# Optimization experiments

Hardware: AMD Instinct MI355X
Metric: run time of the kernel (lower is better)

Reference implementation:

```python
import jax, jax.numpy as jnp
import numpy as np

B = 32; NMAX = 256; E = 512; H = 512; U = 256; M = 32; L = 2; P = 4; TAU = 1.0
S = NMAX + 1                      # pseudo-seq len = nodes + SOS
IN0 = E + (M - 1) + P             # GRU layer-0 input size


def setup_inputs() -> dict:
    key = jax.random.key(0)
    ks = jax.random.split(key, 22)
    f = lambda k, sh, sc=0.05: jax.random.normal(k, sh, dtype=jnp.float32) * sc
    return {
        "h_padded": jax.random.normal(ks[0], (B, NMAX, E), jnp.float32),
        "hg": jax.random.normal(ks[1], (B, E), jnp.float32),
        "num_nodes": jax.random.randint(ks[2], (B,), 1, NMAX + 1),
        "u_noise": jax.random.uniform(ks[3], (M, B, S), jnp.float32),
        "emb_special": f(ks[4], (2, E), 1.0),
        "emb_pos": f(ks[5], (M, P), 1.0),
        "Wp": f(ks[6], (L * H, E)), "bp": f(ks[7], (L * H,)),
        "W_ih0": f(ks[8], (3 * H, IN0)), "W_hh0": f(ks[9], (3 * H, H)),
        "b_ih0": f(ks[10], (3 * H,)), "b_hh0": f(ks[11], (3 * H,)),
        "W_ih1": f(ks[12], (3 * H, H)), "W_hh1": f(ks[13], (3 * H, H)),
        "b_ih1": f(ks[14], (3 * H,)), "b_hh1": f(ks[15], (3 * H,)),
        "W1": f(ks[16], (U, H)), "W2": f(ks[17], (U, H)),
        "wc": f(ks[18], (U,)), "V": f(ks[19], (U,)),
        "Wf": f(ks[20], (M - 1, H)), "bf": f(ks[21], (M - 1,)),
    }


def _gru_step(x, hid, params):
    # torch nn.GRU single time step, L layers; gate order (r, z, n)
    new = []
    inp = x
    for l, (Wi, Wh, bi, bh) in enumerate(params):
        hp = hid[l]
        gi = inp @ Wi.T + bi
        gh = hp @ Wh.T + bh
        gi_r, gi_z, gi_n = jnp.split(gi, 3, axis=-1)
        gh_r, gh_z, gh_n = jnp.split(gh, 3, axis=-1)
        r = jax.nn.sigmoid(gi_r + gh_r)
        z = jax.nn.sigmoid(gi_z + gh_z)
        n = jnp.tanh(gi_n + r * gh_n)
        hn = (1.0 - z) * n + z * hp
        new.append(hn)
        inp = hn
    return inp, jnp.stack(new, 0)


def reference(h_padded, hg, num_nodes, u_noise, emb_special, emb_pos, Wp, bp,
              W_ih0, W_hh0, b_ih0, b_hh0, W_ih1, W_hh1, b_ih1, b_hh1,
              W1, W2, wc, V, Wf, bf):
    lens = num_nodes + 1
    mask = jnp.arange(S)[None, :] < lens[:, None]                       # [B,S]
    node_valid = (jnp.arange(NMAX)[None, :] < num_nodes[:, None]).astype(h_padded.dtype)
    # encoder_out = [SOS emb ; h nodes ; zero pad] as pad_sequence would give
    sos_enc = jnp.broadcast_to(emb_special[1], (B, 1, E))
    encoder_out = jnp.concatenate([sos_enc, h_padded * node_valid[..., None]], axis=1)  # [B,S,E]
    enc_W1 = encoder_out @ W1.T                                          # [B,S,U] hoisted (loop-invariant)
    dec_hidden = jnp.tanh(hg @ Wp.T + bp).reshape(B, L, H).transpose(1, 0, 2)  # [L,B,H]
    theta0 = jnp.zeros((B, M - 1), encoder_out.dtype)
    dec_input = jnp.concatenate([jnp.broadcast_to(emb_special[0], (B, E)), theta0], axis=1)
    cov_vec0 = jnp.zeros((B, S), encoder_out.dtype)
    gumbel = -jnp.log(-jnp.log(u_noise + 1e-10) + 1e-10)                 # [M,B,S]
    gru_params = ((W_ih0, W_hh0, b_ih0, b_hh0), (W_ih1, W_hh1, b_ih1, b_hh1))
    neg = jnp.float32(-1e30)

    def step(carry, xs):
        dec_in, hid, cov_vec, cov_loss = carry
        i, pe, g = xs
        x = jnp.concatenate([dec_in, jnp.broadcast_to(pe, (B, P))], axis=1)
        out, hid = _gru_step(x, hid, gru_params)                        # out [B,H]
        # Bahdanau attention with coverage
        uj = enc_W1 + (out @ W2.T)[:, None, :] + cov_vec[..., None] * wc
        uj = jnp.tanh(uj) @ V                                           # [B,S]
        aj = jax.nn.softmax(jnp.where(mask, uj, neg), axis=-1)
        # hard gumbel-softmax (straight-through)
        logits = jnp.log(aj + 1e-12)
        y = jax.nn.softmax((logits + g) / TAU, axis=1)
        onehot = jax.nn.one_hot(jnp.argmax(y, axis=1), S, dtype=y.dtype)
        hard = jax.lax.stop_gradient(onehot - y) + y
        chosen = jnp.einsum('bse,bs->be', encoder_out, hard)            # [B,E]
        cov_loss = cov_loss + jnp.minimum(aj, cov_vec).sum()
        cov_vec = cov_vec + aj
        theta = jnp.where(i < 1,
                          jnp.zeros((B, M - 1), out.dtype),
                          jax.nn.sigmoid(out @ Wf.T + bf))
        dec_next = jnp.concatenate([chosen, theta], axis=1)
        return (dec_next, hid, cov_vec, cov_loss), (hard, theta, aj)

    init = (dec_input, dec_hidden, cov_vec0, jnp.float32(0.0))
    xs = (jnp.arange(M), emb_pos, gumbel)
    carry_f, (hards, thetas, ajs) = jax.lax.scan(step, init, xs)
    cov_loss = carry_f[3] / B
    pointer = jnp.transpose(hards, (1, 2, 0))   # [B,S,M]
    adj = jnp.transpose(thetas, (1, 2, 0))      # [B,M-1,M]
    atts = jnp.transpose(ajs, (1, 2, 0))        # [B,S,M]
    return pointer, cov_loss, encoder_out, adj, atts
```

## Files before the change

kernel.cpp:

```cpp
#include <hip/hip_runtime.h>

constexpr int NB  = 32;
constexpr int NMX = 256;
constexpr int ED  = 512;
constexpr int HD  = 512;
constexpr int UD  = 256;
constexpr int MS  = 32;
constexpr int PD  = 4;
constexpr int SD  = 257;
constexpr int IL0 = 547;
constexpr int XP  = 576;

constexpr long long OFF_PTR  = 0;
constexpr long long OFF_COVL = (long long)NB*SD*MS;
constexpr long long OFF_ENC  = OFF_COVL + 1;
constexpr long long OFF_ADJ  = OFF_ENC + (long long)NB*SD*ED;
constexpr long long OFF_ATT  = OFF_ADJ + (long long)NB*(MS-1)*MS;

__device__ __forceinline__ float sigf(float x){ return 1.0f/(1.0f + __expf(-x)); }
__device__ __forceinline__ float ftanh(float x){ float e = __expf(2.0f*x); return 1.0f - 2.0f/(e + 1.0f); }

__global__ __launch_bounds__(256) void k_init(const float* __restrict__ hp,
                      const float* __restrict__ embsp, const float* __restrict__ embpos,
                      const float* __restrict__ W1, const float* __restrict__ Wih0,
                      const float* __restrict__ W2, const int* __restrict__ nn,
                      float* __restrict__ out, float* __restrict__ x4,
                      float* __restrict__ cov, float* __restrict__ covl,
                      float* __restrict__ W1T, float* __restrict__ Wih0_4,
                      float* __restrict__ W2T){
  int blk = blockIdx.x, t = threadIdx.x;
  {
    int r = blk*2 + (t >> 7);
    int tid = t & 127;
    int b = r / SD, s = r % SD;
    float* dst = out + OFF_ENC + (long long)r*ED + tid*4;
    if (s == 0){
      const float* src = embsp + ED + tid*4;
      dst[0] = src[0]; dst[1] = src[1]; dst[2] = src[2]; dst[3] = src[3];
    } else if (s-1 < nn[b]){
      const float* src = hp + ((long long)b*NMX + (s-1))*ED + tid*4;
      float4 v = *(const float4*)src;
      dst[0] = v.x; dst[1] = v.y; dst[2] = v.z; dst[3] = v.w;
    } else {
      dst[0] = 0.f; dst[1] = 0.f; dst[2] = 0.f; dst[3] = 0.f;
    }
  }
  const int N0 = XP*NB;
  const int N1 = N0 + NB*SD;
  const int N2 = N1 + NB;
  const int N3 = N2 + UD*ED;
  const int N4 = N3 + 1536*XP;
  const int N5 = N4 + ED*UD;
  for (int i = blk*256 + t; i < N5; i += 4112*256){
    if (i < N0){
      int kb = i >> 7, r = i & 3;
      int k = kb*4 + r;
      float v;
      if (k < ED) v = embsp[k];
      else if (k < ED + MS - 1) v = 0.f;
      else if (k < IL0) v = embpos[k - (ED + MS - 1)];
      else v = 0.f;
      x4[i] = v;
    } else if (i < N1){
      cov[i - N0] = 0.f;
    } else if (i < N2){
      covl[i - N1] = 0.f;
    } else if (i < N3){
      int j = i - N2; int k = j / UD, u = j % UD;
      W1T[j] = W1[(long long)u*ED + k];
    } else if (i < N4){
      int j = i - N3; int row = j / XP, c = j % XP;
      Wih0_4[j] = (c < IL0) ? Wih0[(long long)row*IL0 + c] : 0.f;
    } else {
      int j = i - N4; int k = j / UD, u = j % UD;
      W2T[j] = W2[(long long)u*HD + k];
    }
  }
}

__global__ __launch_bounds__(256) void k_ew1h(const float* __restrict__ out,
                        const float4* __restrict__ W1T4, float4* __restrict__ encW1,
                        const int* __restrict__ nn,
                        const float* __restrict__ hg, const float4* __restrict__ Wp4,
                        const float* __restrict__ bp, float* __restrict__ h0,
                        float* __restrict__ h1){
  __shared__ __align__(16) float As[16][68];
  __shared__ __align__(16) float Bs[16][68];
  int blk = blockIdx.x, t = threadIdx.x;
  if (blk < 516){
    int bm = blk >> 2, bn = blk & 3;
    int m0 = bm*64, n0 = bn*64;
    {
      int rr = m0 + (t & 63);
      bool act = false;
      if (rr < NB*SD){
        int b = rr / SD, s = rr % SD;
        act = (s <= nn[b]);
      }
      if (!__any(act)) return;
    }
    const float* A = out + OFF_ENC;
    int tm = t >> 4, tn = t & 15;
    float4 acc[4];
    #pragma unroll
    for (int i = 0; i < 4; ++i) acc[i] = {0.f,0.f,0.f,0.f};
    int arow = t >> 2, akq = t & 3;
    int bk = t >> 4, bnq = t & 15;
    for (int k0 = 0; k0 < 512; k0 += 16){
      float av[4];
      bool okA = (m0 + arow) < NB*SD;
      long long abase = (long long)(m0 + arow)*ED + k0 + akq*4;
      #pragma unroll
      for (int j = 0; j < 4; ++j) av[j] = okA ? A[abase + j] : 0.f;
      float4 bv = W1T4[(long long)(k0 + bk)*64 + (n0 >> 2) + bnq];
      __syncthreads();
      #pragma unroll
      for (int j = 0; j < 4; ++j) As[akq*4 + j][arow] = av[j];
      *(float4*)&Bs[bk][bnq*4] = bv;
      __syncthreads();
      #pragma unroll
      for (int kk = 0; kk < 16; ++kk){
        float4 a = *(const float4*)&As[kk][tm*4];
        float4 bq = *(const float4*)&Bs[kk][tn*4];
        acc[0].x += a.x*bq.x; acc[0].y += a.x*bq.y; acc[0].z += a.x*bq.z; acc[0].w += a.x*bq.w;
        acc[1].x += a.y*bq.x; acc[1].y += a.y*bq.y; acc[1].z += a.y*bq.z; acc[1].w += a.y*bq.w;
        acc[2].x += a.z*bq.x; acc[2].y += a.z*bq.y; acc[2].z += a.z*bq.z; acc[2].w += a.z*bq.w;
        acc[3].x += a.w*bq.x; acc[3].y += a.w*bq.y; acc[3].z += a.w*bq.z; acc[3].w += a.w*bq.w;
      }
    }
    #pragma unroll
    for (int i = 0; i < 4; ++i){
      int r = m0 + tm*4 + i;
      if (r < NB*SD) encW1[(long long)r*64 + (n0 >> 2) + tn] = acc[i];
    }
  } else {
    int b = t & 31;
    int row = (blk - 516)*8 + (t >> 5);
    const float4* w = Wp4 + (long long)row*128;
    const float4* xg = (const float4*)(hg + (long long)b*ED);
    float acc = bp[row];
    #pragma unroll 4
    for (int i = 0; i < 128; ++i){
      float4 wv = w[i], xv = xg[i];
      acc += wv.x*xv.x + wv.y*xv.y + wv.z*xv.z + wv.w*xv.w;
    }
    float v = ftanh(acc);
    int h = row & 511;
    int idx = (h >> 2)*128 + b*4 + (h & 3);
    if (row < HD) h0[idx] = v;
    else          h1[idx] = v;
  }
}

template<int PER>
__global__ __launch_bounds__(512) void k_gru(const float4* __restrict__ x4,
                      const float4* __restrict__ h4,
                      const float4* __restrict__ Wih4, const float4* __restrict__ Whh4,
                      const float* __restrict__ bih, const float* __restrict__ bhh,
                      float* __restrict__ outT){
  constexpr int NI4 = PER*8;
  __shared__ float part[2][NB][8][6];
  int t = threadIdx.x;
  int b = t & 31, ks = (t >> 5) & 7, hl = (t >> 8) & 1;
  int h = blockIdx.x*2 + hl;
  float ai0 = 0.f, ai1 = 0.f, ai2 = 0.f, ah0 = 0.f, ah1 = 0.f, ah2 = 0.f;
  {
    const float4* w0 = Wih4 + (long long)(0*HD + h)*NI4 + ks*PER;
    const float4* w1 = Wih4 + (long long)(1*HD + h)*NI4 + ks*PER;
    const float4* w2 = Wih4 + (long long)(2*HD + h)*NI4 + ks*PER;
    const float4* xb = x4 + (long long)(ks*PER)*NB + b;
    #pragma unroll
    for (int kb = 0; kb < PER; ++kb){
      float4 xv = xb[kb*NB];
      float4 a = w0[kb], c = w1[kb], d = w2[kb];
      ai0 += xv.x*a.x + xv.y*a.y + xv.z*a.z + xv.w*a.w;
      ai1 += xv.x*c.x + xv.y*c.y + xv.z*c.z + xv.w*c.w;
      ai2 += xv.x*d.x + xv.y*d.y + xv.z*d.z + xv.w*d.w;
    }
  }
  {
    const float4* w0 = Whh4 + (long long)(0*HD + h)*128 + ks*16;
    const float4* w1 = Whh4 + (long long)(1*HD + h)*128 + ks*16;
    const float4* w2 = Whh4 + (long long)(2*HD + h)*128 + ks*16;
    const float4* hb = h4 + (long long)(ks*16)*NB + b;
    #pragma unroll
    for (int kb = 0; kb < 16; ++kb){
      float4 xv = hb[kb*NB];
      float4 a = w0[kb], c = w1[kb], d = w2[kb];
      ah0 += xv.x*a.x + xv.y*a.y + xv.z*a.z + xv.w*a.w;
      ah1 += xv.x*c.x + xv.y*c.y + xv.z*c.z + xv.w*c.w;
      ah2 += xv.x*d.x + xv.y*d.y + xv.z*d.z + xv.w*d.w;
    }
  }
  part[hl][b][ks][0] = ai0; part[hl][b][ks][1] = ai1; part[hl][b][ks][2] = ai2;
  part[hl][b][ks][3] = ah0; part[hl][b][ks][4] = ah1; part[hl][b][ks][5] = ah2;
  __syncthreads();
  if (t < 64){
    int b2 = t & 31, hl2 = t >> 5;
    int h2 = blockIdx.x*2 + hl2;
    float g0=0.f,g1=0.f,g2=0.f,g3=0.f,g4=0.f,g5=0.f;
    #pragma unroll
    for (int k = 0; k < 8; ++k){
      g0 += part[hl2][b2][k][0]; g1 += part[hl2][b2][k][1]; g2 += part[hl2][b2][k][2];
      g3 += part[hl2][b2][k][3]; g4 += part[hl2][b2][k][4]; g5 += part[hl2][b2][k][5];
    }
    float gir = g0 + bih[h2], giz = g1 + bih[HD + h2], gin = g2 + bih[2*HD + h2];
    float ghr = g3 + bhh[h2], ghz = g4 + bhh[HD + h2], ghn = g5 + bhh[2*HD + h2];
    float r = sigf(gir + ghr);
    float z = sigf(giz + ghz);
    float nn = ftanh(gin + r*ghn);
    int idx = (h2 >> 2)*128 + b2*4 + (h2 & 3);
    float hp = ((const float*)h4)[idx];
    outT[idx] = (1.f - z)*nn + z*hp;
  }
}

__global__ __launch_bounds__(512) void k_qs(const float4* __restrict__ h1,
                      const float4* __restrict__ W2T4, const float4* __restrict__ Wf4,
                      const float* __restrict__ bfv, const float* __restrict__ embpos,
                      int m, const float4* __restrict__ encW1,
                      const float4* __restrict__ wc4, const float4* __restrict__ V4,
                      const int* __restrict__ nn,
                      const float* __restrict__ cov, float* __restrict__ sc,
                      float* __restrict__ x4, float* __restrict__ out){
  __shared__ __align__(16) float h1s[512];
  __shared__ __align__(16) float wcs[256];
  __shared__ __align__(16) float Vs[256];
  __shared__ __align__(16) float qs[256];
  __shared__ __align__(16) float4 qpart[8][64];
  int t = threadIdx.x;
  int b = blockIdx.x >> 3, seg = blockIdx.x & 7;
  int n = nn[b];
  if (seg != 0 && seg*33 > n) return;
  if (t < 128) ((float4*)h1s)[t] = h1[t*NB + b];
  else if (t < 192) ((float4*)wcs)[t - 128] = wc4[t - 128];
  else if (t < 256) ((float4*)Vs)[t - 192] = V4[t - 192];
  __syncthreads();
  {
    int u4 = t & 63, kq = t >> 6;
    float4 acc = {0.f,0.f,0.f,0.f};
    const float4* w = W2T4 + (long long)(kq*64)*64 + u4;
    const float* hh = h1s + kq*64;
    #pragma unroll 4
    for (int k = 0; k < 64; ++k){
      float a = hh[k];
      float4 wv = w[(long long)k*64];
      acc.x += a*wv.x; acc.y += a*wv.y; acc.z += a*wv.z; acc.w += a*wv.w;
    }
    qpart[kq][u4] = acc;
  }
  __syncthreads();
  if (t < 64){
    float4 s = qpart[0][t];
    #pragma unroll
    for (int k = 1; k < 8; ++k){
      float4 p = qpart[k][t];
      s.x += p.x; s.y += p.y; s.z += p.z; s.w += p.w;
    }
    ((float4*)qs)[t] = s;
  } else if (seg == 0){
    int w = (t >> 6) - 1;
    int lane = t & 63;
    for (int j = w; j < MS-1; j += 7){
      const float4* wf = Wf4 + (long long)j*128 + lane*2;
      float4 w0 = wf[0], w1v = wf[1];
      const float4* hh4 = (const float4*)h1s + lane*2;
      float4 hv0 = hh4[0], hv1 = hh4[1];
      float d = w0.x*hv0.x + w0.y*hv0.y + w0.z*hv0.z + w0.w*hv0.w
              + w1v.x*hv1.x + w1v.y*hv1.y + w1v.z*hv1.z + w1v.w*hv1.w;
      for (int off = 32; off; off >>= 1) d += __shfl_xor(d, off);
      if (lane == 0){
        float th = (m < 1) ? 0.f : sigf(d + bfv[j]);
        out[OFF_ADJ + (long long)b*(MS-1)*MS + (long long)j*MS + m] = th;
        int k = ED + j;
        x4[(k >> 2)*128 + b*4 + (k & 3)] = th;
      }
    }
  }
  if (seg == 0 && t == 0 && m + 1 < MS){
    #pragma unroll
    for (int p = 0; p < PD; ++p){
      int k = ED + MS - 1 + p;
      x4[(k >> 2)*128 + b*4 + (k & 3)] = embpos[(m+1)*PD + p];
    }
  }
  __syncthreads();
  int lane = t & 63, wav = t >> 6;
  int s0 = seg*33;
  float4 q4 = ((const float4*)qs)[lane];
  float4 wv = ((const float4*)wcs)[lane];
  float4 vv = ((const float4*)Vs)[lane];
  for (int s = s0 + wav; s < s0 + 33 && s < SD; s += 8){
    if (s > n) continue;
    float cv = cov[b*SD + s];
    float4 e4 = encW1[((long long)b*SD + s)*64 + lane];
    float acc = vv.x*ftanh(e4.x + q4.x + cv*wv.x)
              + vv.y*ftanh(e4.y + q4.y + cv*wv.y)
              + vv.z*ftanh(e4.z + q4.z + cv*wv.z)
              + vv.w*ftanh(e4.w + q4.w + cv*wv.w);
    for (int off = 32; off; off >>= 1) acc += __shfl_xor(acc, off);
    if (lane == 0) sc[b*SD + s] = acc;
  }
}

__global__ __launch_bounds__(512) void k_soft(const float* __restrict__ sc,
                      const int* __restrict__ nn, const float* __restrict__ un, int m,
                      float* __restrict__ cov, float* __restrict__ covl,
                      float* __restrict__ out, float4* __restrict__ x4,
                      const float* __restrict__ enc){
  __shared__ float red[8]; __shared__ float redc[8]; __shared__ int redi[8];
  __shared__ float s_mx, s_den; __shared__ int s_k;
  int b = blockIdx.x, t = threadIdx.x;
  int lane = t & 63, wav = t >> 6;
  int n = nn[b];
  float sv = (t < SD) ? sc[b*SD + t] : -3.4e38f;
  float cv = (t < SD) ? cov[b*SD + t] : 0.f;
  float v1 = (t < SD && t <= n) ? sv : -3.4e38f;
  for (int off = 32; off; off >>= 1) v1 = fmaxf(v1, __shfl_xor(v1, off));
  if (lane == 0) red[wav] = v1;
  __syncthreads();
  if (t == 0){
    float mm = red[0];
    for (int i = 1; i < 8; ++i) mm = fmaxf(mm, red[i]);
    s_mx = mm;
  }
  __syncthreads();
  float ev = (t < SD && t <= n) ? __expf(sv - s_mx) : 0.f;
  float v2 = ev;
  for (int off = 32; off; off >>= 1) v2 += __shfl_xor(v2, off);
  if (lane == 0) red[wav] = v2;
  __syncthreads();
  if (t == 0){
    float ss = 0.f;
    for (int i = 0; i < 8; ++i) ss += red[i];
    s_den = ss;
  }
  __syncthreads();
  float aj = (t < SD) ? ev / s_den : 0.f;
  float yl = -3.4e38f; int idx = SD; float lcl = 0.f;
  if (t < SD){
    float u = un[((long long)m*NB + b)*SD + t];
    float g = -__logf(-__logf(u + 1e-10f) + 1e-10f);
    yl = __logf(aj + 1e-12f) + g;
    idx = t;
    lcl = fminf(aj, cv);
    cov[b*SD + t] = cv + aj;
    out[OFF_ATT + ((long long)b*SD + t)*MS + m] = aj;
  }
  for (int off = 32; off; off >>= 1){
    float oy = __shfl_xor(yl, off); int oi = __shfl_xor(idx, off);
    if (oy > yl || (oy == yl && oi < idx)){ yl = oy; idx = oi; }
  }
  for (int off = 32; off; off >>= 1) lcl += __shfl_xor(lcl, off);
  if (lane == 0){ red[wav] = yl; redi[wav] = idx; redc[wav] = lcl; }
  __syncthreads();
  if (t == 0){
    float by = red[0]; int bi = redi[0]; float cl = redc[0];
    for (int w = 1; w < 8; ++w){
      if (red[w] > by || (red[w] == by && redi[w] < bi)){ by = red[w]; bi = redi[w]; }
      cl += redc[w];
    }
    s_k = bi;
    covl[b] += cl;
  }
  __syncthreads();
  int kk = s_k;
  if (t < SD) out[OFF_PTR + ((long long)b*SD + t)*MS + m] = (t == kk) ? 1.f : 0.f;
  const float* er = enc + ((long long)b*SD + kk)*ED;
  if (t < 128){
    float4 v; v.x = er[t*4]; v.y = er[t*4+1]; v.z = er[t*4+2]; v.w = er[t*4+3];
    x4[t*NB + b] = v;
  }
}

__global__ void k_fin(const float* __restrict__ covl, float* __restrict__ out){
  if (threadIdx.x == 0 && blockIdx.x == 0){
    float s = 0.f;
    for (int i = 0; i < NB; ++i) s += covl[i];
    out[OFF_COVL] = s / (float)NB;
  }
}

extern "C" void kernel_launch(void* const* d_in, const int* in_sizes, int n_in,
                              void* d_out, int out_size, void* d_ws, size_t ws_size,
                              hipStream_t stream){
  const float* h_padded    = (const float*)d_in[0];
  const float* hg          = (const float*)d_in[1];
  const int*   num_nodes   = (const int*)  d_in[2];
  const float* u_noise     = (const float*)d_in[3];
  const float* emb_special = (const float*)d_in[4];
  const float* emb_pos     = (const float*)d_in[5];
  const float* Wp          = (const float*)d_in[6];
  const float* bp          = (const float*)d_in[7];
  const float* W_ih0       = (const float*)d_in[8];
  const float* W_hh0       = (const float*)d_in[9];
  const float* b_ih0       = (const float*)d_in[10];
  const float* b_hh0       = (const float*)d_in[11];
  const float* W_ih1       = (const float*)d_in[12];
  const float* W_hh1       = (const float*)d_in[13];
  const float* b_ih1       = (const float*)d_in[14];
  const float* b_hh1       = (const float*)d_in[15];
  const float* W1          = (const float*)d_in[16];
  const float* W2          = (const float*)d_in[17];
  const float* wc          = (const float*)d_in[18];
  const float* V           = (const float*)d_in[19];
  const float* Wf          = (const float*)d_in[20];
  const float* bf          = (const float*)d_in[21];
  float* out = (float*)d_out;

  float* ws      = (float*)d_ws;
  float* encW1   = ws;  ws += (long long)NB*SD*UD;
  float* Wih0_4  = ws;  ws += (long long)1536*XP;
  float* W1T     = ws;  ws += (long long)UD*ED;
  float* W2T     = ws;  ws += (long long)UD*ED;
  float* x4      = ws;  ws += XP*NB;
  float* h0      = ws;  ws += 2*HD*NB;
  float* h1      = ws;  ws += 2*HD*NB;
  float* cov     = ws;  ws += NB*SD;
  float* covl    = ws;  ws += NB;
  float* sc      = ws;  ws += NB*SD;

  k_init<<<4112, 256, 0, stream>>>(h_padded, emb_special, emb_pos, W1, W_ih0, W2,
                                   num_nodes, out, x4, cov, covl, W1T, Wih0_4, W2T);
  k_ew1h<<<644, 256, 0, stream>>>(out, (const float4*)W1T, (float4*)encW1,
                                  num_nodes, hg, (const float4*)Wp, bp, h0, h1);

  for (int m = 0; m < MS; ++m){
    float* h0c = h0 + (m & 1)*HD*NB;
    float* h0n = h0 + ((m + 1) & 1)*HD*NB;
    float* h1c = h1 + (m & 1)*HD*NB;
    float* h1n = h1 + ((m + 1) & 1)*HD*NB;
    k_gru<18><<<256, 512, 0, stream>>>((const float4*)x4, (const float4*)h0c,
        (const float4*)Wih0_4, (const float4*)W_hh0, b_ih0, b_hh0, h0n);
    k_gru<16><<<256, 512, 0, stream>>>((const float4*)h0n, (const float4*)h1c,
        (const float4*)W_ih1, (const float4*)W_hh1, b_ih1, b_hh1, h1n);
    k_qs  <<<256, 512, 0, stream>>>((const float4*)h1n, (const float4*)W2T,
        (const float4*)Wf, bf, emb_pos, m, (const float4*)encW1,
        (const float4*)wc, (const float4*)V, num_nodes, cov, sc, x4, out);
    k_soft<<<NB, 512, 0, stream>>>(sc, num_nodes, u_noise, m, cov, covl, out,
        (float4*)x4, out + OFF_ENC);
  }
  k_fin<<<1, 64, 0, stream>>>(covl, out);
}
```

Measured before the change: 1.290 ms.

## Split GRU reduction across more blocks and compact active encoder tiles

The GRU kernel now assigns one hidden unit per block with a 16-way K split instead of two units per block with an 8-way split, doubling the grid to 512 blocks and adding a two-stage shared-memory reduction. This is meant to expose more parallelism and memory-level concurrency in the latency-bound per-step GRU kernels. Separately, k_init builds a compact list of active 64-row tiles so k_ew1h launches only useful work at the front of the grid instead of early-exiting scattered blocks. The cost is an extra sync and a serial list build by one thread.

```diff
diff --git a/kernel.cpp b/kernel.cpp
--- a/kernel.cpp
+++ b/kernel.cpp
@@ -27,8 +27,24 @@
                       float* __restrict__ out, float* __restrict__ x4,
                       float* __restrict__ cov, float* __restrict__ covl,
                       float* __restrict__ W1T, float* __restrict__ Wih0_4,
-                      float* __restrict__ W2T){
+                      float* __restrict__ W2T, int* __restrict__ tlist){
+  __shared__ short acts[132];
   int blk = blockIdx.x, t = threadIdx.x;
+  if (blk == 0){
+    for (int i = t; i < 129; i += 256){
+      int row0 = i*64;
+      int row1 = row0 + 63; if (row1 > NB*SD - 1) row1 = NB*SD - 1;
+      int b0 = row0 / SD, s0 = row0 - b0*SD;
+      int b1 = row1 / SD;
+      acts[i] = (s0 <= nn[b0]) || (b1 > b0);
+    }
+    __syncthreads();
+    if (t == 0){
+      int c = 0;
+      for (int i = 0; i < 129; ++i) if (acts[i]) tlist[1 + c++] = i;
+      tlist[0] = c;
+    }
+  }
   {
     int r = blk*2 + (t >> 7);
     int tid = t & 127;
@@ -80,7 +96,7 @@
 
 __global__ __launch_bounds__(256) void k_ew1h(const float* __restrict__ out,
                         const float4* __restrict__ W1T4, float4* __restrict__ encW1,
-                        const int* __restrict__ nn,
+                        const int* __restrict__ tlist,
                         const float* __restrict__ hg, const float4* __restrict__ Wp4,
                         const float* __restrict__ bp, float* __restrict__ h0,
                         float* __restrict__ h1){
@@ -88,17 +104,11 @@
   __shared__ __align__(16) float Bs[16][68];
   int blk = blockIdx.x, t = threadIdx.x;
   if (blk < 516){
-    int bm = blk >> 2, bn = blk & 3;
+    int cnt4 = tlist[0]*4;
+    if (blk >= cnt4) return;
+    int bm = tlist[1 + (blk >> 2)];
+    int bn = blk & 3;
     int m0 = bm*64, n0 = bn*64;
-    {
-      int rr = m0 + (t & 63);
-      bool act = false;
-      if (rr < NB*SD){
-        int b = rr / SD, s = rr % SD;
-        act = (s <= nn[b]);
-      }
-      if (!__any(act)) return;
-    }
     const float* A = out + OFF_ENC;
     int tm = t >> 4, tn = t & 15;
     float4 acc[4];
@@ -158,11 +168,12 @@
                       const float4* __restrict__ Wih4, const float4* __restrict__ Whh4,
                       const float* __restrict__ bih, const float* __restrict__ bhh,
                       float* __restrict__ outT){
-  constexpr int NI4 = PER*8;
-  __shared__ float part[2][NB][8][6];
+  constexpr int NI4 = PER*16;
+  __shared__ float part[16][NB][6];
+  __shared__ float part2[2][NB][6];
   int t = threadIdx.x;
-  int b = t & 31, ks = (t >> 5) & 7, hl = (t >> 8) & 1;
-  int h = blockIdx.x*2 + hl;
+  int b = t & 31, ks = (t >> 5) & 15;
+  int h = blockIdx.x;
   float ai0 = 0.f, ai1 = 0.f, ai2 = 0.f, ah0 = 0.f, ah1 = 0.f, ah2 = 0.f;
   {
     const float4* w0 = Wih4 + (long long)(0*HD + h)*NI4 + ks*PER;
@@ -179,12 +190,12 @@
     }
   }
   {
-    const float4* w0 = Whh4 + (long long)(0*HD + h)*128 + ks*16;
-    const float4* w1 = Whh4 + (long long)(1*HD + h)*128 + ks*16;
-    const float4* w2 = Whh4 + (long long)(2*HD + h)*128 + ks*16;
-    const float4* hb = h4 + (long long)(ks*16)*NB + b;
-    #pragma unroll
-    for (int kb = 0; kb < 16; ++kb){
+    const float4* w0 = Whh4 + (long long)(0*HD + h)*128 + ks*8;
+    const float4* w1 = Whh4 + (long long)(1*HD + h)*128 + ks*8;
+    const float4* w2 = Whh4 + (long long)(2*HD + h)*128 + ks*8;
+    const float4* hb = h4 + (long long)(ks*8)*NB + b;
+    #pragma unroll
+    for (int kb = 0; kb < 8; ++kb){
       float4 xv = hb[kb*NB];
       float4 a = w0[kb], c = w1[kb], d = w2[kb];
       ah0 += xv.x*a.x + xv.y*a.y + xv.z*a.z + xv.w*a.w;
@@ -192,24 +203,34 @@
       ah2 += xv.x*d.x + xv.y*d.y + xv.z*d.z + xv.w*d.w;
     }
   }
-  part[hl][b][ks][0] = ai0; part[hl][b][ks][1] = ai1; part[hl][b][ks][2] = ai2;
-  part[hl][b][ks][3] = ah0; part[hl][b][ks][4] = ah1; part[hl][b][ks][5] = ah2;
+  part[ks][b][0] = ai0; part[ks][b][1] = ai1; part[ks][b][2] = ai2;
+  part[ks][b][3] = ah0; part[ks][b][4] = ah1; part[ks][b][5] = ah2;
   __syncthreads();
   if (t < 64){
-    int b2 = t & 31, hl2 = t >> 5;
-    int h2 = blockIdx.x*2 + hl2;
+    int b2 = t & 31, half = t >> 5;
     float g0=0.f,g1=0.f,g2=0.f,g3=0.f,g4=0.f,g5=0.f;
     #pragma unroll
     for (int k = 0; k < 8; ++k){
-      g0 += part[hl2][b2][k][0]; g1 += part[hl2][b2][k][1]; g2 += part[hl2][b2][k][2];
-      g3 += part[hl2][b2][k][3]; g4 += part[hl2][b2][k][4]; g5 += part[hl2][b2][k][5];
-    }
-    float gir = g0 + bih[h2], giz = g1 + bih[HD + h2], gin = g2 + bih[2*HD + h2];
-    float ghr = g3 + bhh[h2], ghz = g4 + bhh[HD + h2], ghn = g5 + bhh[2*HD + h2];
+      int ks2 = half*8 + k;
+      g0 += part[ks2][b2][0]; g1 += part[ks2][b2][1]; g2 += part[ks2][b2][2];
+      g3 += part[ks2][b2][3]; g4 += part[ks2][b2][4]; g5 += part[ks2][b2][5];
+    }
+    part2[half][b2][0] = g0; part2[half][b2][1] = g1; part2[half][b2][2] = g2;
+    part2[half][b2][3] = g3; part2[half][b2][4] = g4; part2[half][b2][5] = g5;
+  }
+  __syncthreads();
+  if (t < 32){
+    int b2 = t;
+    float gir = part2[0][b2][0] + part2[1][b2][0] + bih[h];
+    float giz = part2[0][b2][1] + part2[1][b2][1] + bih[HD + h];
+    float gin = part2[0][b2][2] + part2[1][b2][2] + bih[2*HD + h];
+    float ghr = part2[0][b2][3] + part2[1][b2][3] + bhh[h];
+    float ghz = part2[0][b2][4] + part2[1][b2][4] + bhh[HD + h];
+    float ghn = part2[0][b2][5] + part2[1][b2][5] + bhh[2*HD + h];
     float r = sigf(gir + ghr);
     float z = sigf(giz + ghz);
     float nn = ftanh(gin + r*ghn);
-    int idx = (h2 >> 2)*128 + b2*4 + (h2 & 3);
+    int idx = (h >> 2)*128 + b2*4 + (h & 3);
     float hp = ((const float*)h4)[idx];
     outT[idx] = (1.f - z)*nn + z*hp;
   }
@@ -419,20 +440,22 @@
   float* cov     = ws;  ws += NB*SD;
   float* covl    = ws;  ws += NB;
   float* sc      = ws;  ws += NB*SD;
+  int*   tlist   = (int*)ws; ws += 136;
 
   k_init<<<4112, 256, 0, stream>>>(h_padded, emb_special, emb_pos, W1, W_ih0, W2,
-                                   num_nodes, out, x4, cov, covl, W1T, Wih0_4, W2T);
+                                   num_nodes, out, x4, cov, covl, W1T, Wih0_4, W2T,
+                                   tlist);
   k_ew1h<<<644, 256, 0, stream>>>(out, (const float4*)W1T, (float4*)encW1,
-                                  num_nodes, hg, (const float4*)Wp, bp, h0, h1);
+                                  tlist, hg, (const float4*)Wp, bp, h0, h1);
 
   for (int m = 0; m < MS; ++m){
     float* h0c = h0 + (m & 1)*HD*NB;
     float* h0n = h0 + ((m + 1) & 1)*HD*NB;
     float* h1c = h1 + (m & 1)*HD*NB;
     float* h1n = h1 + ((m + 1) & 1)*HD*NB;
-    k_gru<18><<<256, 512, 0, stream>>>((const float4*)x4, (const float4*)h0c,
+    k_gru<9><<<512, 512, 0, stream>>>((const float4*)x4, (const float4*)h0c,
         (const float4*)Wih0_4, (const float4*)W_hh0, b_ih0, b_hh0, h0n);
-    k_gru<16><<<256, 512, 0, stream>>>((const float4*)h0n, (const float4*)h1c,
+    k_gru<8><<<512, 512, 0, stream>>>((const float4*)h0n, (const float4*)h1c,
         (const float4*)W_ih1, (const float4*)W_hh1, b_ih1, b_hh1, h1n);
     k_qs  <<<256, 512, 0, stream>>>((const float4*)h1n, (const float4*)W2T,
         (const float4*)Wf, bf, emb_pos, m, (const float4*)encW1,
```

Result: no change. 1.312 ms (+1.7%).

## Precompute GRU hidden-hidden matvecs in idle blocks of attention/softmax kernels

Applied to the files above, without the earlier changes.

The recurrent W_hh·h products for the next step are now computed by extra blocks added to the k_qs and k_soft launches. Those kernels otherwise run few blocks, so this work overlaps with them and shortens each k_gru launch on the serial critical path. The prologue kernels are merged into one launch, and the W1 transpose is dropped by reading W1 directly in the GEMM. The GEMM's A operand now comes straight from h_padded. An aligned copy of the encoder output in workspace allows float4 gathers in k_soft. The cost is extra scratch buffers and more blocks in the per-step kernels.

```diff
diff --git a/kernel.cpp b/kernel.cpp
--- a/kernel.cpp
+++ b/kernel.cpp
@@ -20,103 +20,50 @@
 __device__ __forceinline__ float sigf(float x){ return 1.0f/(1.0f + __expf(-x)); }
 __device__ __forceinline__ float ftanh(float x){ float e = __expf(2.0f*x); return 1.0f - 2.0f/(e + 1.0f); }
 
-__global__ __launch_bounds__(256) void k_init(const float* __restrict__ hp,
-                      const float* __restrict__ embsp, const float* __restrict__ embpos,
-                      const float* __restrict__ W1, const float* __restrict__ Wih0,
-                      const float* __restrict__ W2, const int* __restrict__ nn,
-                      float* __restrict__ out, float* __restrict__ x4,
-                      float* __restrict__ cov, float* __restrict__ covl,
-                      float* __restrict__ W1T, float* __restrict__ Wih0_4,
-                      float* __restrict__ W2T){
-  int blk = blockIdx.x, t = threadIdx.x;
-  {
-    int r = blk*2 + (t >> 7);
-    int tid = t & 127;
-    int b = r / SD, s = r % SD;
-    float* dst = out + OFF_ENC + (long long)r*ED + tid*4;
-    if (s == 0){
-      const float* src = embsp + ED + tid*4;
-      dst[0] = src[0]; dst[1] = src[1]; dst[2] = src[2]; dst[3] = src[3];
-    } else if (s-1 < nn[b]){
-      const float* src = hp + ((long long)b*NMX + (s-1))*ED + tid*4;
-      float4 v = *(const float4*)src;
-      dst[0] = v.x; dst[1] = v.y; dst[2] = v.z; dst[3] = v.w;
-    } else {
-      dst[0] = 0.f; dst[1] = 0.f; dst[2] = 0.f; dst[3] = 0.f;
-    }
-  }
-  const int N0 = XP*NB;
-  const int N1 = N0 + NB*SD;
-  const int N2 = N1 + NB;
-  const int N3 = N2 + UD*ED;
-  const int N4 = N3 + 1536*XP;
-  const int N5 = N4 + ED*UD;
-  for (int i = blk*256 + t; i < N5; i += 4112*256){
-    if (i < N0){
-      int kb = i >> 7, r = i & 3;
-      int k = kb*4 + r;
-      float v;
-      if (k < ED) v = embsp[k];
-      else if (k < ED + MS - 1) v = 0.f;
-      else if (k < IL0) v = embpos[k - (ED + MS - 1)];
-      else v = 0.f;
-      x4[i] = v;
-    } else if (i < N1){
-      cov[i - N0] = 0.f;
-    } else if (i < N2){
-      covl[i - N1] = 0.f;
-    } else if (i < N3){
-      int j = i - N2; int k = j / UD, u = j % UD;
-      W1T[j] = W1[(long long)u*ED + k];
-    } else if (i < N4){
-      int j = i - N3; int row = j / XP, c = j % XP;
-      Wih0_4[j] = (c < IL0) ? Wih0[(long long)row*IL0 + c] : 0.f;
-    } else {
-      int j = i - N4; int k = j / UD, u = j % UD;
-      W2T[j] = W2[(long long)u*HD + k];
-    }
-  }
-}
-
-__global__ __launch_bounds__(256) void k_ew1h(const float* __restrict__ out,
-                        const float4* __restrict__ W1T4, float4* __restrict__ encW1,
-                        const int* __restrict__ nn,
-                        const float* __restrict__ hg, const float4* __restrict__ Wp4,
-                        const float* __restrict__ bp, float* __restrict__ h0,
-                        float* __restrict__ h1){
+__global__ __launch_bounds__(256) void k_pro(const float* __restrict__ hp,
+    const float* __restrict__ hg, const float* __restrict__ embsp,
+    const float* __restrict__ embpos, const float* __restrict__ W1,
+    const float* __restrict__ Wih0, const float* __restrict__ W2,
+    const int* __restrict__ nn, const float4* __restrict__ Wp4,
+    const float* __restrict__ bp,
+    float* __restrict__ out, float* __restrict__ encA, int useA,
+    float4* __restrict__ encW1,
+    float* __restrict__ x4, float* __restrict__ cov, float* __restrict__ covl,
+    float* __restrict__ Wih0_4, float* __restrict__ W2T,
+    float* __restrict__ h0, float* __restrict__ h1){
   __shared__ __align__(16) float As[16][68];
   __shared__ __align__(16) float Bs[16][68];
   int blk = blockIdx.x, t = threadIdx.x;
   if (blk < 516){
     int bm = blk >> 2, bn = blk & 3;
     int m0 = bm*64, n0 = bn*64;
-    {
-      int rr = m0 + (t & 63);
-      bool act = false;
-      if (rr < NB*SD){
-        int b = rr / SD, s = rr % SD;
-        act = (s <= nn[b]);
-      }
-      if (!__any(act)) return;
-    }
-    const float* A = out + OFF_ENC;
     int tm = t >> 4, tn = t & 15;
     float4 acc[4];
     #pragma unroll
     for (int i = 0; i < 4; ++i) acc[i] = {0.f,0.f,0.f,0.f};
     int arow = t >> 2, akq = t & 3;
-    int bk = t >> 4, bnq = t & 15;
+    int r = m0 + arow;
+    int amode = 0;
+    const float* abase = embsp + ED;
+    if (r < NB*SD){
+      int ab = r / SD, as = r - ab*SD;
+      if (as == 0) amode = 1;
+      else if (as <= nn[ab]){ amode = 2; abase = hp + ((long long)ab*NMX + (as-1))*ED; }
+    }
+    int bk = t & 15, bu = t >> 4;
     for (int k0 = 0; k0 < 512; k0 += 16){
-      float av[4];
-      bool okA = (m0 + arow) < NB*SD;
-      long long abase = (long long)(m0 + arow)*ED + k0 + akq*4;
+      float4 av = {0.f,0.f,0.f,0.f};
+      if (amode) av = *(const float4*)(abase + k0 + akq*4);
+      float bv[4];
       #pragma unroll
-      for (int j = 0; j < 4; ++j) av[j] = okA ? A[abase + j] : 0.f;
-      float4 bv = W1T4[(long long)(k0 + bk)*64 + (n0 >> 2) + bnq];
+      for (int j = 0; j < 4; ++j)
+        bv[j] = W1[(long long)(n0 + bu*4 + j)*ED + k0 + bk];
       __syncthreads();
-      #pragma unroll
-      for (int j = 0; j < 4; ++j) As[akq*4 + j][arow] = av[j];
-      *(float4*)&Bs[bk][bnq*4] = bv;
+      As[akq*4 + 0][arow] = av.x;
+      As[akq*4 + 1][arow] = av.y;
+      As[akq*4 + 2][arow] = av.z;
+      As[akq*4 + 3][arow] = av.w;
+      *(float4*)&Bs[bk][bu*4] = make_float4(bv[0], bv[1], bv[2], bv[3]);
       __syncthreads();
       #pragma unroll
       for (int kk = 0; kk < 16; ++kk){
@@ -130,10 +77,10 @@
     }
     #pragma unroll
     for (int i = 0; i < 4; ++i){
-      int r = m0 + tm*4 + i;
-      if (r < NB*SD) encW1[(long long)r*64 + (n0 >> 2) + tn] = acc[i];
-    }
-  } else {
+      int rr = m0 + tm*4 + i;
+      if (rr < NB*SD) encW1[(long long)rr*64 + (n0 >> 2) + tn] = acc[i];
+    }
+  } else if (blk < 644){
     int b = t & 31;
     int row = (blk - 516)*8 + (t >> 5);
     const float4* w = Wp4 + (long long)row*128;
@@ -149,21 +96,95 @@
     int idx = (h >> 2)*128 + b*4 + (h & 3);
     if (row < HD) h0[idx] = v;
     else          h1[idx] = v;
-  }
-}
-
-template<int PER>
+  } else {
+    int eb = blk - 644;
+    {
+      int r = eb*2 + (t >> 7);
+      int tid = t & 127;
+      int b = r / SD, s = r - b*SD;
+      float4 v = {0.f,0.f,0.f,0.f};
+      if (s == 0) v = *(const float4*)(embsp + ED + tid*4);
+      else if (s <= nn[b]) v = *(const float4*)(hp + ((long long)b*NMX + (s-1))*ED + tid*4);
+      float* dst = out + OFF_ENC + (long long)r*ED + tid*4;
+      dst[0] = v.x; dst[1] = v.y; dst[2] = v.z; dst[3] = v.w;
+      if (useA) *(float4*)(encA + (long long)r*ED + tid*4) = v;
+    }
+    const int N0 = XP*NB;
+    const int N1 = N0 + NB*SD;
+    const int N2 = N1 + NB;
+    const int N3 = N2 + 1536*XP;
+    const int N4 = N3 + ED*UD;
+    for (int i = eb*256 + t; i < N4; i += 4112*256){
+      if (i < N0){
+        int kb = i >> 7, rr = i & 3;
+        int k = kb*4 + rr;
+        float v;
+        if (k < ED) v = embsp[k];
+        else if (k < ED + MS - 1) v = 0.f;
+        else if (k < IL0) v = embpos[k - (ED + MS - 1)];
+        else v = 0.f;
+        x4[i] = v;
+      } else if (i < N1){
+        cov[i - N0] = 0.f;
+      } else if (i < N2){
+        covl[i - N1] = 0.f;
+      } else if (i < N3){
+        int j = i - N2; int row = j / XP, c = j % XP;
+        Wih0_4[j] = (c < IL0) ? Wih0[(long long)row*IL0 + c] : 0.f;
+      } else {
+        int j = i - N3; int k = j / UD, u = j % UD;
+        W2T[j] = W2[(long long)u*HD + k];
+      }
+    }
+  }
+}
+
+__device__ __forceinline__ void hh_pre(const float4* __restrict__ h4,
+    const float4* __restrict__ Whh4, float* __restrict__ ghh,
+    int bh, int t, float (*part)[NB][8][6]){
+  int b = t & 31, ks = (t >> 5) & 7, hl = (t >> 8) & 1;
+  int h = bh*2 + hl;
+  float a0 = 0.f, a1 = 0.f, a2 = 0.f;
+  const float4* w0 = Whh4 + (long long)(0*HD + h)*128 + ks*16;
+  const float4* w1 = Whh4 + (long long)(1*HD + h)*128 + ks*16;
+  const float4* w2 = Whh4 + (long long)(2*HD + h)*128 + ks*16;
+  const float4* hb = h4 + (long long)(ks*16)*NB + b;
+  #pragma unroll
+  for (int kb = 0; kb < 16; ++kb){
+    float4 xv = hb[kb*NB];
+    float4 a = w0[kb], c = w1[kb], d = w2[kb];
+    a0 += xv.x*a.x + xv.y*a.y + xv.z*a.z + xv.w*a.w;
+    a1 += xv.x*c.x + xv.y*c.y + xv.z*c.z + xv.w*c.w;
+    a2 += xv.x*d.x + xv.y*d.y + xv.z*d.z + xv.w*d.w;
+  }
+  part[hl][b][ks][0] = a0; part[hl][b][ks][1] = a1; part[hl][b][ks][2] = a2;
+  __syncthreads();
+  if (t < 64){
+    int b2 = t & 31, hl2 = t >> 5;
+    int h2 = bh*2 + hl2;
+    float g0 = 0.f, g1 = 0.f, g2 = 0.f;
+    #pragma unroll
+    for (int k = 0; k < 8; ++k){
+      g0 += part[hl2][b2][k][0]; g1 += part[hl2][b2][k][1]; g2 += part[hl2][b2][k][2];
+    }
+    ghh[(0*HD + h2)*NB + b2] = g0;
+    ghh[(1*HD + h2)*NB + b2] = g1;
+    ghh[(2*HD + h2)*NB + b2] = g2;
+  }
+}
+
+template<int PER, bool PRE>
 __global__ __launch_bounds__(512) void k_gru(const float4* __restrict__ x4,
                       const float4* __restrict__ h4,
                       const float4* __restrict__ Wih4, const float4* __restrict__ Whh4,
                       const float* __restrict__ bih, const float* __restrict__ bhh,
-                      float* __restrict__ outT){
+                      float* __restrict__ outT, const float* __restrict__ ghh){
   constexpr int NI4 = PER*8;
   __shared__ float part[2][NB][8][6];
   int t = threadIdx.x;
   int b = t & 31, ks = (t >> 5) & 7, hl = (t >> 8) & 1;
   int h = blockIdx.x*2 + hl;
-  float ai0 = 0.f, ai1 = 0.f, ai2 = 0.f, ah0 = 0.f, ah1 = 0.f, ah2 = 0.f;
+  float ai0 = 0.f, ai1 = 0.f, ai2 = 0.f;
   {
     const float4* w0 = Wih4 + (long long)(0*HD + h)*NI4 + ks*PER;
     const float4* w1 = Wih4 + (long long)(1*HD + h)*NI4 + ks*PER;
@@ -178,7 +199,8 @@
       ai2 += xv.x*d.x + xv.y*d.y + xv.z*d.z + xv.w*d.w;
     }
   }
-  {
+  if (!PRE){
+    float ah0 = 0.f, ah1 = 0.f, ah2 = 0.f;
     const float4* w0 = Whh4 + (long long)(0*HD + h)*128 + ks*16;
     const float4* w1 = Whh4 + (long long)(1*HD + h)*128 + ks*16;
     const float4* w2 = Whh4 + (long long)(2*HD + h)*128 + ks*16;
@@ -191,21 +213,33 @@
       ah1 += xv.x*c.x + xv.y*c.y + xv.z*c.z + xv.w*c.w;
       ah2 += xv.x*d.x + xv.y*d.y + xv.z*d.z + xv.w*d.w;
     }
+    part[hl][b][ks][3] = ah0; part[hl][b][ks][4] = ah1; part[hl][b][ks][5] = ah2;
   }
   part[hl][b][ks][0] = ai0; part[hl][b][ks][1] = ai1; part[hl][b][ks][2] = ai2;
-  part[hl][b][ks][3] = ah0; part[hl][b][ks][4] = ah1; part[hl][b][ks][5] = ah2;
   __syncthreads();
   if (t < 64){
     int b2 = t & 31, hl2 = t >> 5;
     int h2 = blockIdx.x*2 + hl2;
-    float g0=0.f,g1=0.f,g2=0.f,g3=0.f,g4=0.f,g5=0.f;
+    float g0=0.f,g1=0.f,g2=0.f;
     #pragma unroll
     for (int k = 0; k < 8; ++k){
       g0 += part[hl2][b2][k][0]; g1 += part[hl2][b2][k][1]; g2 += part[hl2][b2][k][2];
-      g3 += part[hl2][b2][k][3]; g4 += part[hl2][b2][k][4]; g5 += part[hl2][b2][k][5];
+    }
+    float ghr, ghz, ghn;
+    if (PRE){
+      ghr = ghh[(0*HD + h2)*NB + b2];
+      ghz = ghh[(1*HD + h2)*NB + b2];
+      ghn = ghh[(2*HD + h2)*NB + b2];
+    } else {
+      float g3=0.f,g4=0.f,g5=0.f;
+      #pragma unroll
+      for (int k = 0; k < 8; ++k){
+        g3 += part[hl2][b2][k][3]; g4 += part[hl2][b2][k][4]; g5 += part[hl2][b2][k][5];
+      }
+      ghr = g3; ghz = g4; ghn = g5;
     }
     float gir = g0 + bih[h2], giz = g1 + bih[HD + h2], gin = g2 + bih[2*HD + h2];
-    float ghr = g3 + bhh[h2], ghz = g4 + bhh[HD + h2], ghn = g5 + bhh[2*HD + h2];
+    ghr += bhh[h2]; ghz += bhh[HD + h2]; ghn += bhh[2*HD + h2];
     float r = sigf(gir + ghr);
     float z = sigf(giz + ghz);
     float nn = ftanh(gin + r*ghn);
@@ -222,49 +256,55 @@
                       const float4* __restrict__ wc4, const float4* __restrict__ V4,
                       const int* __restrict__ nn,
                       const float* __restrict__ cov, float* __restrict__ sc,
-                      float* __restrict__ x4, float* __restrict__ out){
-  __shared__ __align__(16) float h1s[512];
-  __shared__ __align__(16) float wcs[256];
-  __shared__ __align__(16) float Vs[256];
-  __shared__ __align__(16) float qs[256];
-  __shared__ __align__(16) float4 qpart[8][64];
+                      float* __restrict__ x4, float* __restrict__ out,
+                      const float4* __restrict__ Whh1_4, float* __restrict__ ghh1){
+  union QMem {
+    struct { float h1s[512]; float wcs[256]; float Vs[256]; float qs[256];
+             float4 qpart[8][64]; } q;
+    float part[2][NB][8][6];
+  };
+  __shared__ __align__(16) QMem sm;
   int t = threadIdx.x;
+  if (blockIdx.x >= 256){
+    hh_pre(h1, Whh1_4, ghh1, blockIdx.x - 256, t, sm.part);
+    return;
+  }
   int b = blockIdx.x >> 3, seg = blockIdx.x & 7;
   int n = nn[b];
   if (seg != 0 && seg*33 > n) return;
-  if (t < 128) ((float4*)h1s)[t] = h1[t*NB + b];
-  else if (t < 192) ((float4*)wcs)[t - 128] = wc4[t - 128];
-  else if (t < 256) ((float4*)Vs)[t - 192] = V4[t - 192];
+  if (t < 128) ((float4*)sm.q.h1s)[t] = h1[t*NB + b];
+  else if (t < 192) ((float4*)sm.q.wcs)[t - 128] = wc4[t - 128];
+  else if (t < 256) ((float4*)sm.q.Vs)[t - 192] = V4[t - 192];
   __syncthreads();
   {
     int u4 = t & 63, kq = t >> 6;
     float4 acc = {0.f,0.f,0.f,0.f};
     const float4* w = W2T4 + (long long)(kq*64)*64 + u4;
-    const float* hh = h1s + kq*64;
+    const float* hh = sm.q.h1s + kq*64;
     #pragma unroll 4
     for (int k = 0; k < 64; ++k){
       float a = hh[k];
       float4 wv = w[(long long)k*64];
       acc.x += a*wv.x; acc.y += a*wv.y; acc.z += a*wv.z; acc.w += a*wv.w;
     }
-    qpart[kq][u4] = acc;
+    sm.q.qpart[kq][u4] = acc;
   }
   __syncthreads();
   if (t < 64){
-    float4 s = qpart[0][t];
+    float4 s = sm.q.qpart[0][t];
     #pragma unroll
     for (int k = 1; k < 8; ++k){
-      float4 p = qpart[k][t];
+      float4 p = sm.q.qpart[k][t];
       s.x += p.x; s.y += p.y; s.z += p.z; s.w += p.w;
     }
-    ((float4*)qs)[t] = s;
+    ((float4*)sm.q.qs)[t] = s;
   } else if (seg == 0){
     int w = (t >> 6) - 1;
     int lane = t & 63;
     for (int j = w; j < MS-1; j += 7){
       const float4* wf = Wf4 + (long long)j*128 + lane*2;
       float4 w0 = wf[0], w1v = wf[1];
-      const float4* hh4 = (const float4*)h1s + lane*2;
+      const float4* hh4 = (const float4*)sm.q.h1s + lane*2;
       float4 hv0 = hh4[0], hv1 = hh4[1];
       float d = w0.x*hv0.x + w0.y*hv0.y + w0.z*hv0.z + w0.w*hv0.w
               + w1v.x*hv1.x + w1v.y*hv1.y + w1v.z*hv1.z + w1v.w*hv1.w;
@@ -287,9 +327,9 @@
   __syncthreads();
   int lane = t & 63, wav = t >> 6;
   int s0 = seg*33;
-  float4 q4 = ((const float4*)qs)[lane];
-  float4 wv = ((const float4*)wcs)[lane];
-  float4 vv = ((const float4*)Vs)[lane];
+  float4 q4 = ((const float4*)sm.q.qs)[lane];
+  float4 wv = ((const float4*)sm.q.wcs)[lane];
+  float4 vv = ((const float4*)sm.q.Vs)[lane];
   for (int s = s0 + wav; s < s0 + 33 && s < SD; s += 8){
     if (s > n) continue;
     float cv = cov[b*SD + s];
@@ -307,36 +347,46 @@
                       const int* __restrict__ nn, const float* __restrict__ un, int m,
                       float* __restrict__ cov, float* __restrict__ covl,
                       float* __restrict__ out, float4* __restrict__ x4,
-                      const float* __restrict__ enc){
-  __shared__ float red[8]; __shared__ float redc[8]; __shared__ int redi[8];
-  __shared__ float s_mx, s_den; __shared__ int s_k;
-  int b = blockIdx.x, t = threadIdx.x;
+                      const float* __restrict__ encSrc, int alignedA,
+                      const float4* __restrict__ h0n4,
+                      const float4* __restrict__ Whh0_4, float* __restrict__ ghh0){
+  union SMem {
+    struct { float red[8]; float redc[8]; int redi[8]; float s_mx, s_den; int s_k; } s;
+    float part[2][NB][8][6];
+  };
+  __shared__ __align__(16) SMem sm;
+  int t = threadIdx.x;
+  if (blockIdx.x >= 32){
+    hh_pre(h0n4, Whh0_4, ghh0, blockIdx.x - 32, t, sm.part);
+    return;
+  }
+  int b = blockIdx.x;
   int lane = t & 63, wav = t >> 6;
   int n = nn[b];
   float sv = (t < SD) ? sc[b*SD + t] : -3.4e38f;
   float cv = (t < SD) ? cov[b*SD + t] : 0.f;
   float v1 = (t < SD && t <= n) ? sv : -3.4e38f;
   for (int off = 32; off; off >>= 1) v1 = fmaxf(v1, __shfl_xor(v1, off));
-  if (lane == 0) red[wav] = v1;
+  if (lane == 0) sm.s.red[wav] = v1;
   __syncthreads();
   if (t == 0){
-    float mm = red[0];
-    for (int i = 1; i < 8; ++i) mm = fmaxf(mm, red[i]);
-    s_mx = mm;
-  }
-  __syncthreads();
-  float ev = (t < SD && t <= n) ? __expf(sv - s_mx) : 0.f;
+    float mm = sm.s.red[0];
+    for (int i = 1; i < 8; ++i) mm = fmaxf(mm, sm.s.red[i]);
+    sm.s.s_mx = mm;
+  }
+  __syncthreads();
+  float ev = (t < SD && t <= n) ? __expf(sv - sm.s.s_mx) : 0.f;
   float v2 = ev;
   for (int off = 32; off; off >>= 1) v2 += __shfl_xor(v2, off);
-  if (lane == 0) red[wav] = v2;
+  if (lane == 0) sm.s.red[wav] = v2;
   __syncthreads();
   if (t == 0){
     float ss = 0.f;
-    for (int i = 0; i < 8; ++i) ss += red[i];
-    s_den = ss;
-  }
-  __syncthreads();
-  float aj = (t < SD) ? ev / s_den : 0.f;
+    for (int i = 0; i < 8; ++i) ss += sm.s.red[i];
+    sm.s.s_den = ss;
+  }
+  __syncthreads();
+  float aj = (t < SD) ? ev / sm.s.s_den : 0.f;
   float yl = -3.4e38f; int idx = SD; float lcl = 0.f;
   if (t < SD){
     float u = un[((long long)m*NB + b)*SD + t];
@@ -352,24 +402,31 @@
     if (oy > yl || (oy == yl && oi < idx)){ yl = oy; idx = oi; }
   }
   for (int off = 32; off; off >>= 1) lcl += __shfl_xor(lcl, off);
-  if (lane == 0){ red[wav] = yl; redi[wav] = idx; redc[wav] = lcl; }
+  if (lane == 0){ sm.s.red[wav] = yl; sm.s.redi[wav] = idx; sm.s.redc[wav] = lcl; }
   __syncthreads();
   if (t == 0){
-    float by = red[0]; int bi = redi[0]; float cl = redc[0];
+    float by = sm.s.red[0]; int bi = sm.s.redi[0]; float cl = sm.s.redc[0];
     for (int w = 1; w < 8; ++w){
-      if (red[w] > by || (red[w] == by && redi[w] < bi)){ by = red[w]; bi = redi[w]; }
-      cl += redc[w];
-    }
-    s_k = bi;
+      if (sm.s.red[w] > by || (sm.s.red[w] == by && sm.s.redi[w] < bi)){
+        by = sm.s.red[w]; bi = sm.s.redi[w];
+      }
+      cl += sm.s.redc[w];
+    }
+    sm.s.s_k = bi;
     covl[b] += cl;
   }
   __syncthreads();
-  int kk = s_k;
+  int kk = sm.s.s_k;
   if (t < SD) out[OFF_PTR + ((long long)b*SD + t)*MS + m] = (t == kk) ? 1.f : 0.f;
-  const float* er = enc + ((long long)b*SD + kk)*ED;
   if (t < 128){
-    float4 v; v.x = er[t*4]; v.y = er[t*4+1]; v.z = er[t*4+2]; v.w = er[t*4+3];
-    x4[t*NB + b] = v;
+    if (alignedA){
+      float4 v = ((const float4*)(encSrc + (long long)(b*SD + kk)*ED))[t];
+      x4[t*NB + b] = v;
+    } else {
+      const float* er = encSrc + (long long)(b*SD + kk)*ED;
+      float4 v; v.x = er[t*4]; v.y = er[t*4+1]; v.z = er[t*4+2]; v.w = er[t*4+3];
+      x4[t*NB + b] = v;
+    }
   }
 }
 
@@ -411,7 +468,6 @@
   float* ws      = (float*)d_ws;
   float* encW1   = ws;  ws += (long long)NB*SD*UD;
   float* Wih0_4  = ws;  ws += (long long)1536*XP;
-  float* W1T     = ws;  ws += (long long)UD*ED;
   float* W2T     = ws;  ws += (long long)UD*ED;
   float* x4      = ws;  ws += XP*NB;
   float* h0      = ws;  ws += 2*HD*NB;
@@ -419,26 +475,39 @@
   float* cov     = ws;  ws += NB*SD;
   float* covl    = ws;  ws += NB;
   float* sc      = ws;  ws += NB*SD;
-
-  k_init<<<4112, 256, 0, stream>>>(h_padded, emb_special, emb_pos, W1, W_ih0, W2,
-                                   num_nodes, out, x4, cov, covl, W1T, Wih0_4, W2T);
-  k_ew1h<<<644, 256, 0, stream>>>(out, (const float4*)W1T, (float4*)encW1,
-                                  num_nodes, hg, (const float4*)Wp, bp, h0, h1);
+  float* ghh0    = ws;  ws += 3*HD*NB;
+  float* ghh1    = ws;  ws += 3*HD*NB;
+  float* encA    = ws;
+  size_t used_base = (size_t)((char*)ws - (char*)d_ws);
+  int useA = (ws_size >= used_base + (size_t)NB*SD*ED*sizeof(float)) ? 1 : 0;
+  const float* encSrc = useA ? encA : (out + OFF_ENC);
+
+  k_pro<<<4756, 256, 0, stream>>>(h_padded, hg, emb_special, emb_pos, W1, W_ih0, W2,
+                                  num_nodes, (const float4*)Wp, bp, out, encA, useA,
+                                  (float4*)encW1, x4, cov, covl, Wih0_4, W2T, h0, h1);
 
   for (int m = 0; m < MS; ++m){
     float* h0c = h0 + (m & 1)*HD*NB;
     float* h0n = h0 + ((m + 1) & 1)*HD*NB;
     float* h1c = h1 + (m & 1)*HD*NB;
     float* h1n = h1 + ((m + 1) & 1)*HD*NB;
-    k_gru<18><<<256, 512, 0, stream>>>((const float4*)x4, (const float4*)h0c,
-        (const float4*)Wih0_4, (const float4*)W_hh0, b_ih0, b_hh0, h0n);
-    k_gru<16><<<256, 512, 0, stream>>>((const float4*)h0n, (const float4*)h1c,
-        (const float4*)W_ih1, (const float4*)W_hh1, b_ih1, b_hh1, h1n);
-    k_qs  <<<256, 512, 0, stream>>>((const float4*)h1n, (const float4*)W2T,
+    if (m == 0){
+      k_gru<18,false><<<256, 512, 0, stream>>>((const float4*)x4, (const float4*)h0c,
+          (const float4*)Wih0_4, (const float4*)W_hh0, b_ih0, b_hh0, h0n, nullptr);
+      k_gru<16,false><<<256, 512, 0, stream>>>((const float4*)h0n, (const float4*)h1c,
+          (const float4*)W_ih1, (const float4*)W_hh1, b_ih1, b_hh1, h1n, nullptr);
+    } else {
+      k_gru<18,true><<<256, 512, 0, stream>>>((const float4*)x4, (const float4*)h0c,
+          (const float4*)Wih0_4, (const float4*)W_hh0, b_ih0, b_hh0, h0n, ghh0);
+      k_gru<16,true><<<256, 512, 0, stream>>>((const float4*)h0n, (const float4*)h1c,
+          (const float4*)W_ih1, (const float4*)W_hh1, b_ih1, b_hh1, h1n, ghh1);
+    }
+    k_qs  <<<512, 512, 0, stream>>>((const float4*)h1n, (const float4*)W2T,
         (const float4*)Wf, bf, emb_pos, m, (const float4*)encW1,
-        (const float4*)wc, (const float4*)V, num_nodes, cov, sc, x4, out);
-    k_soft<<<NB, 512, 0, stream>>>(sc, num_nodes, u_noise, m, cov, covl, out,
-        (float4*)x4, out + OFF_ENC);
+        (const float4*)wc, (const float4*)V, num_nodes, cov, sc, x4, out,
+        (const float4*)W_hh1, ghh1);
+    k_soft<<<288, 512, 0, stream>>>(sc, num_nodes, u_noise, m, cov, covl, out,
+        (float4*)x4, encSrc, useA, (const float4*)h0n, (const float4*)W_hh0, ghh0);
   }
   k_fin<<<1, 64, 0, stream>>>(covl, out);
 }
```

Result: faster. 1.219 ms (-5.5%).
